# Optimization experiments

Measured on AMD Instinct MI355X. Metric: run time of the kernel, lower is better.

The kernel has to match this reference:

```python
import jax, jax.numpy as jnp
import numpy as np

N_NODES = 100000
N_EDGES = 1250000
D = 64  # in_dim == hid_dim (same Linear reused by both SSGConv layers)


def setup_inputs() -> dict:
    key = jax.random.key(0)
    k1, k2, k3, k4 = jax.random.split(key, 4)
    x = jax.random.normal(k1, (N_NODES, D), dtype=jnp.float32)
    edge_index = jax.random.randint(k2, (2, N_EDGES), 0, N_NODES, dtype=jnp.int64)
    W1 = jax.random.normal(k3, (D, D), dtype=jnp.float32) * (1.0 / np.sqrt(D))
    b1 = jax.random.normal(k4, (D,), dtype=jnp.float32) * 0.01
    return {"x": x, "edge_index": edge_index, "W1": W1, "b1": b1}


def reference(x, edge_index, W1, b1):
    # SSGConv(nn1): sum-aggregate neighbor features over edge_index, then Linear.
    src = edge_index[0]
    dst = edge_index[1]
    n = x.shape[0]

    def ssg_conv(h):
        # gather source-node features per edge, scatter-add into destinations
        agg = jax.ops.segment_sum(h[src], dst, num_segments=n)  # [N, D]
        return agg @ W1.T + b1  # shared nn1 for both layers (faithful to source)

    hid = ssg_conv(x)
    out = ssg_conv(hid)
    return (out, hid)
```

## Files before the change

### kernel.cpp

```cpp
#include <hip/hip_runtime.h>

#define N_NODES 100000
#define N_EDGES 1250000
#define D 64

#define BSHIFT 9
#define BUCKETS 196
#define CAP 8192
#define CHUNK 4096
#define PA_BLOCKS ((N_EDGES + CHUNK - 1) / CHUNK)
#define CVT_BLOCKS 718
#define LCAP 64

typedef long long ll;
typedef unsigned int uint;

__device__ __forceinline__ ushort f2bf(float f) {
    uint u = __float_as_uint(f);
    u += 0x7fffu + ((u >> 16) & 1u);
    return (ushort)(u >> 16);
}

__global__ void init_kernel(int* __restrict__ cursor, int* __restrict__ srt,
                            int* __restrict__ offs) {
    int t = threadIdx.x;
    if (t < BUCKETS) cursor[t] = t * CAP;
    if (t < 8) srt[N_EDGES + t] = 0;
    if (t == 0) offs[N_NODES] = N_EDGES;
}

__global__ __launch_bounds__(512) void bucketA_cvt_kernel(const int* __restrict__ src,
                                                          const int* __restrict__ dst,
                                                          int* __restrict__ cursor,
                                                          int* __restrict__ tmp,
                                                          const float* __restrict__ x,
                                                          ushort* __restrict__ xb) {
    int tid = threadIdx.x;
    if (blockIdx.x >= PA_BLOCKS) {
        const int n4 = N_NODES * D / 4;
        int i = (blockIdx.x - PA_BLOCKS) * 512 + tid;
        const int stride = CVT_BLOCKS * 512;
        for (; i < n4; i += stride) {
            float4 v = ((const float4*)x)[i];
            ushort4 o;
            o.x = f2bf(v.x); o.y = f2bf(v.y); o.z = f2bf(v.z); o.w = f2bf(v.w);
            ((ushort4*)xb)[i] = o;
        }
        return;
    }

    __shared__ int lcnt[BUCKETS];
    __shared__ int gbs[BUCKETS];
    __shared__ int list[BUCKETS * LCAP];
    if (tid < BUCKETS) lcnt[tid] = 0;
    __syncthreads();

    int base = blockIdx.x * CHUNK;
    int nE = min(CHUNK, N_EDGES - base);
    for (int i = tid; i < nE; i += 512) {
        int e = base + i;
        int s = src[e], d = dst[e];
        int b = d >> BSHIFT;
        int p = atomicAdd(&lcnt[b], 1);
        list[b * LCAP + p] = s | ((d & 511) << 17);
    }
    __syncthreads();

    if (tid < BUCKETS) gbs[tid] = atomicAdd(&cursor[tid], lcnt[tid]);
    __syncthreads();

    int wv = tid >> 6, lane = tid & 63;
    for (int b = wv; b < BUCKETS; b += 8) {
        int c = lcnt[b];
        if (lane < c) tmp[gbs[b] + lane] = list[b * LCAP + lane];
    }
}

__global__ __launch_bounds__(512) void bucketB_kernel(const int* __restrict__ cursor,
                                                      const int* __restrict__ tmp,
                                                      int* __restrict__ srt,
                                                      int* __restrict__ offs) {
    __shared__ int hist[512];
    __shared__ int cur[512];
    __shared__ int sbase[256];
    __shared__ int wsum[8];
    const int b = blockIdx.x, tid = threadIdx.x;
    const int wv = tid >> 6, lane = tid & 63;
    const int cbase = b * CAP;
    const int cnt = cursor[b] - cbase;

    hist[tid] = 0;
    if (wv == 0) {
        int c0, c1, c2, c3;
        const int b4 = lane << 2;
        c0 = (b4     < BUCKETS) ? (cursor[b4]     - (b4    ) * CAP) : 0;
        c1 = (b4 + 1 < BUCKETS) ? (cursor[b4 + 1] - (b4 + 1) * CAP) : 0;
        c2 = (b4 + 2 < BUCKETS) ? (cursor[b4 + 2] - (b4 + 2) * CAP) : 0;
        c3 = (b4 + 3 < BUCKETS) ? (cursor[b4 + 3] - (b4 + 3) * CAP) : 0;
        const int s1 = c0 + c1, sum = s1 + c2 + c3;
        int run = sum;
#pragma unroll
        for (int d = 1; d < 64; d <<= 1) {
            int t = __shfl_up(run, d);
            if (lane >= d) run += t;
        }
        const int lex = run - sum;
        sbase[b4]     = lex;
        sbase[b4 + 1] = lex + c0;
        sbase[b4 + 2] = lex + s1;
        sbase[b4 + 3] = lex + s1 + c2;
    }
    __syncthreads();
    const int gbase = sbase[b];

    for (int i = tid; i < cnt; i += 512) {
        int ln = tmp[cbase + i] >> 17;
        atomicAdd(&hist[ln], 1);
    }
    __syncthreads();

    const int x = hist[tid];
    int v = x;
#pragma unroll
    for (int d = 1; d < 64; d <<= 1) {
        int t = __shfl_up(v, d);
        if (lane >= d) v += t;
    }
    if (lane == 63) wsum[wv] = v;
    __syncthreads();
    int woff = 0;
#pragma unroll
    for (int k = 0; k < 8; ++k) woff += (k < wv) ? wsum[k] : 0;
    const int excl = v + woff - x;
    cur[tid] = excl;

    const int node0 = b << BSHIFT;
    const int nloc = min(512, N_NODES - node0);
    if (tid < nloc) offs[node0 + tid] = gbase + excl;
    __syncthreads();

    for (int i = tid; i < cnt; i += 512) {
        int t = tmp[cbase + i];
        int ln = t >> 17;
        int p = atomicAdd(&cur[ln], 1);
        srt[gbase + p] = t & 0x1FFFF;
    }
}

#define NBLK 2048
#define ACC4(P, M, AX, AY, AZ, AW)                        \
    {                                                     \
        float f0 = __uint_as_float((P).x << 16);          \
        float f1 = __uint_as_float((P).x & 0xffff0000u);  \
        float f2 = __uint_as_float((P).y << 16);          \
        float f3 = __uint_as_float((P).y & 0xffff0000u);  \
        AX = fmaf(f0, (M), AX); AY = fmaf(f1, (M), AY);   \
        AZ = fmaf(f2, (M), AZ); AW = fmaf(f3, (M), AW);   \
    }

template<int EMIT>
__global__ __launch_bounds__(256) void fused_layer(const ushort* __restrict__ hb,
                                                   const int* __restrict__ offs,
                                                   const int* __restrict__ srt,
                                                   const float* __restrict__ W1,
                                                   const float* __restrict__ b1,
                                                   float* __restrict__ out,
                                                   ushort* __restrict__ outb) {
    __shared__ __align__(16) float rbA[4][64];
    __shared__ __align__(16) float rbB[4][64];
    const int tid  = threadIdx.x;
    const int lane = tid & 63;
    const int wid  = tid >> 6;
    const int g    = lane >> 4;
    const int sub  = lane & 15;
    const uint roff = (uint)sub << 3;
    const int gw   = blockIdx.x * 4 + wid;
    const int GW   = NBLK * 4;
    const int goff = g << 2;
    const char* hbase = (const char*)hb;

    const float4* wrow = (const float4*)(W1 + lane * D);
    const float bj = b1[lane];

    for (int p = gw; p < (N_NODES >> 1); p += GW) {
        const int nA = p << 1;
        const int2 o2 = *(const int2*)(offs + nA);
        const int begA = o2.x;
        const int endA = o2.y;
        const int endB = offs[nA + 2];
        const int emA = (endA > begA) ? endA - 1 : begA;
        const int emB = (endB > endA) ? endB - 1 : endA;

        float aAx = 0.f, aAy = 0.f, aAz = 0.f, aAw = 0.f;
        float aBx = 0.f, aBy = 0.f, aBz = 0.f, aBw = 0.f;

        int ebA = begA, ebB = endA;
        while (ebA < endA || ebB < endB) {
            const int eA = ebA + goff;
            const int eB = ebB + goff;
            const int cA0 = min(eA,     emA), cA1 = min(eA + 1, emA);
            const int cA2 = min(eA + 2, emA), cA3 = min(eA + 3, emA);
            const int cB0 = min(eB,     emB), cB1 = min(eB + 1, emB);
            const int cB2 = min(eB + 2, emB), cB3 = min(eB + 3, emB);
            const int sA0 = srt[cA0];
            const int sA1 = srt[cA1];
            const int sA2 = srt[cA2];
            const int sA3 = srt[cA3];
            const int sB0 = srt[cB0];
            const int sB1 = srt[cB1];
            const int sB2 = srt[cB2];
            const int sB3 = srt[cB3];
            const uint2 vA0 = *(const uint2*)(hbase + (((uint)sA0 << 7) + roff));
            const uint2 vA1 = *(const uint2*)(hbase + (((uint)sA1 << 7) + roff));
            const uint2 vA2 = *(const uint2*)(hbase + (((uint)sA2 << 7) + roff));
            const uint2 vA3 = *(const uint2*)(hbase + (((uint)sA3 << 7) + roff));
            const uint2 vB0 = *(const uint2*)(hbase + (((uint)sB0 << 7) + roff));
            const uint2 vB1 = *(const uint2*)(hbase + (((uint)sB1 << 7) + roff));
            const uint2 vB2 = *(const uint2*)(hbase + (((uint)sB2 << 7) + roff));
            const uint2 vB3 = *(const uint2*)(hbase + (((uint)sB3 << 7) + roff));
            const float mA0 = (eA     < endA) ? 1.f : 0.f;
            const float mA1 = (eA + 1 < endA) ? 1.f : 0.f;
            const float mA2 = (eA + 2 < endA) ? 1.f : 0.f;
            const float mA3 = (eA + 3 < endA) ? 1.f : 0.f;
            const float mB0 = (eB     < endB) ? 1.f : 0.f;
            const float mB1 = (eB + 1 < endB) ? 1.f : 0.f;
            const float mB2 = (eB + 2 < endB) ? 1.f : 0.f;
            const float mB3 = (eB + 3 < endB) ? 1.f : 0.f;
            ACC4(vA0, mA0, aAx, aAy, aAz, aAw);
            ACC4(vA1, mA1, aAx, aAy, aAz, aAw);
            ACC4(vA2, mA2, aAx, aAy, aAz, aAw);
            ACC4(vA3, mA3, aAx, aAy, aAz, aAw);
            ACC4(vB0, mB0, aBx, aBy, aBz, aBw);
            ACC4(vB1, mB1, aBx, aBy, aBz, aBw);
            ACC4(vB2, mB2, aBx, aBy, aBz, aBw);
            ACC4(vB3, mB3, aBx, aBy, aBz, aBw);
            ebA += 16; ebB += 16;
        }

        aAx += __shfl_xor(aAx, 16); aAy += __shfl_xor(aAy, 16);
        aAz += __shfl_xor(aAz, 16); aAw += __shfl_xor(aAw, 16);
        aBx += __shfl_xor(aBx, 16); aBy += __shfl_xor(aBy, 16);
        aBz += __shfl_xor(aBz, 16); aBw += __shfl_xor(aBw, 16);
        aAx += __shfl_xor(aAx, 32); aAy += __shfl_xor(aAy, 32);
        aAz += __shfl_xor(aAz, 32); aAw += __shfl_xor(aAw, 32);
        aBx += __shfl_xor(aBx, 32); aBy += __shfl_xor(aBy, 32);
        aBz += __shfl_xor(aBz, 32); aBw += __shfl_xor(aBw, 32);

        if (g == 0) {
            float4 t; t.x = aAx; t.y = aAy; t.z = aAz; t.w = aAw;
            *((float4*)rbA[wid] + sub) = t;
        }
        if (g == 1) {
            float4 t; t.x = aBx; t.y = aBy; t.z = aBz; t.w = aBw;
            *((float4*)rbB[wid] + sub) = t;
        }

        float oA = bj, oB = bj;
        const float4* ra = (const float4*)rbA[wid];
        const float4* rb = (const float4*)rbB[wid];
#pragma unroll
        for (int k4 = 0; k4 < 16; ++k4) {
            const float4 w  = wrow[k4];
            const float4 rA = ra[k4];
            const float4 rB = rb[k4];
            oA += rA.x * w.x + rA.y * w.y + rA.z * w.z + rA.w * w.w;
            oB += rB.x * w.x + rB.y * w.y + rB.z * w.z + rB.w * w.w;
        }
        __builtin_nontemporal_store(oA, out + (ll)nA * D + lane);
        __builtin_nontemporal_store(oB, out + (ll)(nA + 1) * D + lane);
        if (EMIT) {
            outb[(ll)nA * D + lane]       = f2bf(oA);
            outb[(ll)(nA + 1) * D + lane] = f2bf(oB);
        }
    }
}

extern "C" void kernel_launch(void* const* d_in, const int* in_sizes, int n_in,
                              void* d_out, int out_size, void* d_ws, size_t ws_size,
                              hipStream_t stream) {
    const float* x  = (const float*)d_in[0];
    const int* edge = (const int*)d_in[1];
    const float* W1 = (const float*)d_in[2];
    const float* b1 = (const float*)d_in[3];

    const int* src = edge;
    const int* dst = edge + N_EDGES;

    float* out = (float*)d_out;
    float* hid = (float*)d_out + (ll)N_NODES * D;

    ushort* xb = (ushort*)d_out;

    char* ws = (char*)d_ws;
    int* cursor   = (int*)ws;  ws += 1024;
    int* offs     = (int*)ws;  ws += ((size_t)(N_NODES + 1) * 4 + 255) & ~255ull;
    int* srt      = (int*)ws;  ws += ((size_t)(N_EDGES + 8) * 4 + 255) & ~255ull;
    ushort* hidb  = (ushort*)ws; ws += (size_t)N_NODES * D * 2;
    int* tmp      = (int*)ws;

    init_kernel<<<1, 256, 0, stream>>>(cursor, srt, offs);
    bucketA_cvt_kernel<<<PA_BLOCKS + CVT_BLOCKS, 512, 0, stream>>>(src, dst, cursor,
                                                                   tmp, x, xb);
    bucketB_kernel<<<BUCKETS, 512, 0, stream>>>(cursor, tmp, srt, offs);

    fused_layer<1><<<NBLK, 256, 0, stream>>>(xb, offs, srt, W1, b1, hid, hidb);
    fused_layer<0><<<NBLK, 256, 0, stream>>>(hidb, offs, srt, W1, b1, out, (ushort*)nullptr);
}
```

Baseline: 230.4 us.

## Replace two-pass bucket sort with degree-count CSR padded to multiples of 16

```diff
diff --git a/kernel.cpp b/kernel.cpp
--- a/kernel.cpp
+++ b/kernel.cpp
@@ -6,11 +6,11 @@
 
 #define BSHIFT 9
 #define BUCKETS 196
-#define CAP 8192
-#define CHUNK 4096
-#define PA_BLOCKS ((N_EDGES + CHUNK - 1) / CHUNK)
+#define PAD_CAP 2400000
+#define CNT_BLOCKS 640
 #define CVT_BLOCKS 718
-#define LCAP 64
+#define SC_BLOCKS 1280
+#define NBLK 2048
 
 typedef long long ll;
 typedef unsigned int uint;
@@ -21,26 +21,32 @@
     return (ushort)(u >> 16);
 }
 
-__global__ void init_kernel(int* __restrict__ cursor, int* __restrict__ srt,
-                            int* __restrict__ offs) {
-    int t = threadIdx.x;
-    if (t < BUCKETS) cursor[t] = t * CAP;
-    if (t < 8) srt[N_EDGES + t] = 0;
-    if (t == 0) offs[N_NODES] = N_EDGES;
-}
-
-__global__ __launch_bounds__(512) void bucketA_cvt_kernel(const int* __restrict__ src,
-                                                          const int* __restrict__ dst,
-                                                          int* __restrict__ cursor,
-                                                          int* __restrict__ tmp,
-                                                          const float* __restrict__ x,
-                                                          ushort* __restrict__ xb) {
-    int tid = threadIdx.x;
-    if (blockIdx.x >= PA_BLOCKS) {
+__global__ __launch_bounds__(256) void prep_kernel(int* __restrict__ deg,
+                                                   int* __restrict__ srt,
+                                                   ushort* __restrict__ xb,
+                                                   ushort* __restrict__ hidb) {
+    const int i0 = blockIdx.x * 256 + threadIdx.x;
+    const int stride = gridDim.x * 256;
+    const int4 f4 = make_int4(N_NODES, N_NODES, N_NODES, N_NODES);
+    for (int i = i0; i < (PAD_CAP + 64) / 4; i += stride) ((int4*)srt)[i] = f4;
+    const int4 z4 = make_int4(0, 0, 0, 0);
+    for (int i = i0; i < N_NODES / 4; i += stride) ((int4*)deg)[i] = z4;
+    if (i0 < 16) {
+        uint2 z; z.x = 0; z.y = 0;
+        ((uint2*)(xb   + (ll)N_NODES * D))[i0] = z;
+        ((uint2*)(hidb + (ll)N_NODES * D))[i0] = z;
+    }
+}
+
+__global__ __launch_bounds__(512) void count_cvt_kernel(const int* __restrict__ dst,
+                                                        int* __restrict__ deg,
+                                                        const float* __restrict__ x,
+                                                        ushort* __restrict__ xb) {
+    const int tid = threadIdx.x;
+    if (blockIdx.x >= CNT_BLOCKS) {
         const int n4 = N_NODES * D / 4;
-        int i = (blockIdx.x - PA_BLOCKS) * 512 + tid;
-        const int stride = CVT_BLOCKS * 512;
-        for (; i < n4; i += stride) {
+        int i = (blockIdx.x - CNT_BLOCKS) * 512 + tid;
+        for (; i < n4; i += CVT_BLOCKS * 512) {
             float4 v = ((const float4*)x)[i];
             ushort4 o;
             o.x = f2bf(v.x); o.y = f2bf(v.y); o.z = f2bf(v.z); o.w = f2bf(v.w);
@@ -48,55 +54,47 @@
         }
         return;
     }
-
-    __shared__ int lcnt[BUCKETS];
-    __shared__ int gbs[BUCKETS];
-    __shared__ int list[BUCKETS * LCAP];
-    if (tid < BUCKETS) lcnt[tid] = 0;
+    int i = blockIdx.x * 512 + tid;
+    for (; i < N_EDGES; i += CNT_BLOCKS * 512) atomicAdd(&deg[dst[i]], 1);
+}
+
+__global__ __launch_bounds__(512) void degscan1_kernel(const int* __restrict__ deg,
+                                                       int* __restrict__ bsum) {
+    const int b = blockIdx.x, tid = threadIdx.x;
+    const int lane = tid & 63, wv = tid >> 6;
+    const int node0 = b << BSHIFT;
+    const int nloc = min(512, N_NODES - node0);
+    int pd = 0;
+    if (tid < nloc) pd = (deg[node0 + tid] + 15) & ~15;
+    int v = pd;
+#pragma unroll
+    for (int d = 1; d < 64; d <<= 1) v += __shfl_xor(v, d);
+    __shared__ int ws[8];
+    if (lane == 0) ws[wv] = v;
     __syncthreads();
-
-    int base = blockIdx.x * CHUNK;
-    int nE = min(CHUNK, N_EDGES - base);
-    for (int i = tid; i < nE; i += 512) {
-        int e = base + i;
-        int s = src[e], d = dst[e];
-        int b = d >> BSHIFT;
-        int p = atomicAdd(&lcnt[b], 1);
-        list[b * LCAP + p] = s | ((d & 511) << 17);
-    }
-    __syncthreads();
-
-    if (tid < BUCKETS) gbs[tid] = atomicAdd(&cursor[tid], lcnt[tid]);
-    __syncthreads();
-
-    int wv = tid >> 6, lane = tid & 63;
-    for (int b = wv; b < BUCKETS; b += 8) {
-        int c = lcnt[b];
-        if (lane < c) tmp[gbs[b] + lane] = list[b * LCAP + lane];
-    }
-}
-
-__global__ __launch_bounds__(512) void bucketB_kernel(const int* __restrict__ cursor,
-                                                      const int* __restrict__ tmp,
-                                                      int* __restrict__ srt,
-                                                      int* __restrict__ offs) {
-    __shared__ int hist[512];
-    __shared__ int cur[512];
+    if (tid == 0) {
+        int s = 0;
+#pragma unroll
+        for (int k = 0; k < 8; ++k) s += ws[k];
+        bsum[b] = s;
+    }
+}
+
+__global__ __launch_bounds__(512) void degscan2_kernel(const int* __restrict__ deg,
+                                                       const int* __restrict__ bsum,
+                                                       int* __restrict__ offs,
+                                                       int* __restrict__ cur) {
     __shared__ int sbase[256];
     __shared__ int wsum[8];
+    __shared__ int tot;
     const int b = blockIdx.x, tid = threadIdx.x;
-    const int wv = tid >> 6, lane = tid & 63;
-    const int cbase = b * CAP;
-    const int cnt = cursor[b] - cbase;
-
-    hist[tid] = 0;
+    const int lane = tid & 63, wv = tid >> 6;
     if (wv == 0) {
-        int c0, c1, c2, c3;
         const int b4 = lane << 2;
-        c0 = (b4     < BUCKETS) ? (cursor[b4]     - (b4    ) * CAP) : 0;
-        c1 = (b4 + 1 < BUCKETS) ? (cursor[b4 + 1] - (b4 + 1) * CAP) : 0;
-        c2 = (b4 + 2 < BUCKETS) ? (cursor[b4 + 2] - (b4 + 2) * CAP) : 0;
-        c3 = (b4 + 3 < BUCKETS) ? (cursor[b4 + 3] - (b4 + 3) * CAP) : 0;
+        int c0 = (b4     < BUCKETS) ? bsum[b4]     : 0;
+        int c1 = (b4 + 1 < BUCKETS) ? bsum[b4 + 1] : 0;
+        int c2 = (b4 + 2 < BUCKETS) ? bsum[b4 + 2] : 0;
+        int c3 = (b4 + 3 < BUCKETS) ? bsum[b4 + 3] : 0;
         const int s1 = c0 + c1, sum = s1 + c2 + c3;
         int run = sum;
 #pragma unroll
@@ -109,18 +107,14 @@
         sbase[b4 + 1] = lex + c0;
         sbase[b4 + 2] = lex + s1;
         sbase[b4 + 3] = lex + s1 + c2;
+        if (lane == 63) tot = run;
     }
     __syncthreads();
     const int gbase = sbase[b];
-
-    for (int i = tid; i < cnt; i += 512) {
-        int ln = tmp[cbase + i] >> 17;
-        atomicAdd(&hist[ln], 1);
-    }
-    __syncthreads();
-
-    const int x = hist[tid];
-    int v = x;
+    const int node0 = b << BSHIFT;
+    const int nloc = min(512, N_NODES - node0);
+    int pd = (tid < nloc) ? ((deg[node0 + tid] + 15) & ~15) : 0;
+    int v = pd;
 #pragma unroll
     for (int d = 1; d < 64; d <<= 1) {
         int t = __shfl_up(v, d);
@@ -131,32 +125,31 @@
     int woff = 0;
 #pragma unroll
     for (int k = 0; k < 8; ++k) woff += (k < wv) ? wsum[k] : 0;
-    const int excl = v + woff - x;
-    cur[tid] = excl;
-
-    const int node0 = b << BSHIFT;
-    const int nloc = min(512, N_NODES - node0);
-    if (tid < nloc) offs[node0 + tid] = gbase + excl;
-    __syncthreads();
-
-    for (int i = tid; i < cnt; i += 512) {
-        int t = tmp[cbase + i];
-        int ln = t >> 17;
-        int p = atomicAdd(&cur[ln], 1);
-        srt[gbase + p] = t & 0x1FFFF;
-    }
-}
-
-#define NBLK 2048
-#define ACC4(P, M, AX, AY, AZ, AW)                        \
-    {                                                     \
-        float f0 = __uint_as_float((P).x << 16);          \
-        float f1 = __uint_as_float((P).x & 0xffff0000u);  \
-        float f2 = __uint_as_float((P).y << 16);          \
-        float f3 = __uint_as_float((P).y & 0xffff0000u);  \
-        AX = fmaf(f0, (M), AX); AY = fmaf(f1, (M), AY);   \
-        AZ = fmaf(f2, (M), AZ); AW = fmaf(f3, (M), AW);   \
-    }
+    const int excl = v + woff - pd;
+    if (tid < nloc) {
+        offs[node0 + tid] = gbase + excl;
+        cur[node0 + tid]  = gbase + excl;
+    }
+    if (b == BUCKETS - 1 && tid == 0) offs[N_NODES] = tot;
+}
+
+__global__ __launch_bounds__(256) void scatter_kernel(const int* __restrict__ src,
+                                                      const int* __restrict__ dst,
+                                                      int* __restrict__ cur,
+                                                      int* __restrict__ srt) {
+    int i = blockIdx.x * 256 + threadIdx.x;
+    for (; i < N_EDGES; i += SC_BLOCKS * 256) {
+        int d = dst[i], s = src[i];
+        int p = atomicAdd(&cur[d], 1);
+        srt[p] = s;
+    }
+}
+
+#define UACC(V, AX, AY, AZ, AW)                               \
+    AX += __uint_as_float((V).x << 16);                       \
+    AY += __uint_as_float((V).x & 0xffff0000u);               \
+    AZ += __uint_as_float((V).y << 16);                       \
+    AW += __uint_as_float((V).y & 0xffff0000u);
 
 template<int EMIT>
 __global__ __launch_bounds__(256) void fused_layer(const ushort* __restrict__ hb,
@@ -174,9 +167,9 @@
     const int g    = lane >> 4;
     const int sub  = lane & 15;
     const uint roff = (uint)sub << 3;
+    const int goff = g << 2;
     const int gw   = blockIdx.x * 4 + wid;
     const int GW   = NBLK * 4;
-    const int goff = g << 2;
     const char* hbase = (const char*)hb;
 
     const float4* wrow = (const float4*)(W1 + lane * D);
@@ -188,52 +181,38 @@
         const int begA = o2.x;
         const int endA = o2.y;
         const int endB = offs[nA + 2];
-        const int emA = (endA > begA) ? endA - 1 : begA;
-        const int emB = (endB > endA) ? endB - 1 : endA;
 
         float aAx = 0.f, aAy = 0.f, aAz = 0.f, aAw = 0.f;
         float aBx = 0.f, aBy = 0.f, aBz = 0.f, aBw = 0.f;
 
         int ebA = begA, ebB = endA;
         while (ebA < endA || ebB < endB) {
-            const int eA = ebA + goff;
-            const int eB = ebB + goff;
-            const int cA0 = min(eA,     emA), cA1 = min(eA + 1, emA);
-            const int cA2 = min(eA + 2, emA), cA3 = min(eA + 3, emA);
-            const int cB0 = min(eB,     emB), cB1 = min(eB + 1, emB);
-            const int cB2 = min(eB + 2, emB), cB3 = min(eB + 3, emB);
-            const int sA0 = srt[cA0];
-            const int sA1 = srt[cA1];
-            const int sA2 = srt[cA2];
-            const int sA3 = srt[cA3];
-            const int sB0 = srt[cB0];
-            const int sB1 = srt[cB1];
-            const int sB2 = srt[cB2];
-            const int sB3 = srt[cB3];
-            const uint2 vA0 = *(const uint2*)(hbase + (((uint)sA0 << 7) + roff));
-            const uint2 vA1 = *(const uint2*)(hbase + (((uint)sA1 << 7) + roff));
-            const uint2 vA2 = *(const uint2*)(hbase + (((uint)sA2 << 7) + roff));
-            const uint2 vA3 = *(const uint2*)(hbase + (((uint)sA3 << 7) + roff));
-            const uint2 vB0 = *(const uint2*)(hbase + (((uint)sB0 << 7) + roff));
-            const uint2 vB1 = *(const uint2*)(hbase + (((uint)sB1 << 7) + roff));
-            const uint2 vB2 = *(const uint2*)(hbase + (((uint)sB2 << 7) + roff));
-            const uint2 vB3 = *(const uint2*)(hbase + (((uint)sB3 << 7) + roff));
-            const float mA0 = (eA     < endA) ? 1.f : 0.f;
-            const float mA1 = (eA + 1 < endA) ? 1.f : 0.f;
-            const float mA2 = (eA + 2 < endA) ? 1.f : 0.f;
-            const float mA3 = (eA + 3 < endA) ? 1.f : 0.f;
-            const float mB0 = (eB     < endB) ? 1.f : 0.f;
-            const float mB1 = (eB + 1 < endB) ? 1.f : 0.f;
-            const float mB2 = (eB + 2 < endB) ? 1.f : 0.f;
-            const float mB3 = (eB + 3 < endB) ? 1.f : 0.f;
-            ACC4(vA0, mA0, aAx, aAy, aAz, aAw);
-            ACC4(vA1, mA1, aAx, aAy, aAz, aAw);
-            ACC4(vA2, mA2, aAx, aAy, aAz, aAw);
-            ACC4(vA3, mA3, aAx, aAy, aAz, aAw);
-            ACC4(vB0, mB0, aBx, aBy, aBz, aBw);
-            ACC4(vB1, mB1, aBx, aBy, aBz, aBw);
-            ACC4(vB2, mB2, aBx, aBy, aBz, aBw);
-            ACC4(vB3, mB3, aBx, aBy, aBz, aBw);
+            int siA = (ebA < endA) ? srt[ebA + sub] : N_NODES;
+            int siB = (ebB < endB) ? srt[ebB + sub] : N_NODES;
+            const int iA0 = __shfl(siA, goff);
+            const int iA1 = __shfl(siA, goff + 1);
+            const int iA2 = __shfl(siA, goff + 2);
+            const int iA3 = __shfl(siA, goff + 3);
+            const int iB0 = __shfl(siB, goff);
+            const int iB1 = __shfl(siB, goff + 1);
+            const int iB2 = __shfl(siB, goff + 2);
+            const int iB3 = __shfl(siB, goff + 3);
+            const uint2 vA0 = *(const uint2*)(hbase + (((uint)iA0 << 7) + roff));
+            const uint2 vA1 = *(const uint2*)(hbase + (((uint)iA1 << 7) + roff));
+            const uint2 vA2 = *(const uint2*)(hbase + (((uint)iA2 << 7) + roff));
+            const uint2 vA3 = *(const uint2*)(hbase + (((uint)iA3 << 7) + roff));
+            const uint2 vB0 = *(const uint2*)(hbase + (((uint)iB0 << 7) + roff));
+            const uint2 vB1 = *(const uint2*)(hbase + (((uint)iB1 << 7) + roff));
+            const uint2 vB2 = *(const uint2*)(hbase + (((uint)iB2 << 7) + roff));
+            const uint2 vB3 = *(const uint2*)(hbase + (((uint)iB3 << 7) + roff));
+            UACC(vA0, aAx, aAy, aAz, aAw);
+            UACC(vA1, aAx, aAy, aAz, aAw);
+            UACC(vA2, aAx, aAy, aAz, aAw);
+            UACC(vA3, aAx, aAy, aAz, aAw);
+            UACC(vB0, aBx, aBy, aBz, aBw);
+            UACC(vB1, aBx, aBy, aBz, aBw);
+            UACC(vB2, aBx, aBy, aBz, aBw);
+            UACC(vB3, aBx, aBy, aBz, aBw);
             ebA += 16; ebB += 16;
         }
 
@@ -292,16 +271,18 @@
     ushort* xb = (ushort*)d_out;
 
     char* ws = (char*)d_ws;
-    int* cursor   = (int*)ws;  ws += 1024;
-    int* offs     = (int*)ws;  ws += ((size_t)(N_NODES + 1) * 4 + 255) & ~255ull;
-    int* srt      = (int*)ws;  ws += ((size_t)(N_EDGES + 8) * 4 + 255) & ~255ull;
-    ushort* hidb  = (ushort*)ws; ws += (size_t)N_NODES * D * 2;
-    int* tmp      = (int*)ws;
-
-    init_kernel<<<1, 256, 0, stream>>>(cursor, srt, offs);
-    bucketA_cvt_kernel<<<PA_BLOCKS + CVT_BLOCKS, 512, 0, stream>>>(src, dst, cursor,
-                                                                   tmp, x, xb);
-    bucketB_kernel<<<BUCKETS, 512, 0, stream>>>(cursor, tmp, srt, offs);
+    int* deg    = (int*)ws;  ws += ((size_t)N_NODES * 4 + 255) & ~255ull;
+    int* cur    = (int*)ws;  ws += ((size_t)N_NODES * 4 + 255) & ~255ull;
+    int* offs   = (int*)ws;  ws += ((size_t)(N_NODES + 1) * 4 + 255) & ~255ull;
+    int* bsum   = (int*)ws;  ws += 1024;
+    int* srt    = (int*)ws;  ws += ((size_t)(PAD_CAP + 64) * 4 + 255) & ~255ull;
+    ushort* hidb = (ushort*)ws;
+
+    prep_kernel<<<1024, 256, 0, stream>>>(deg, srt, xb, hidb);
+    count_cvt_kernel<<<CNT_BLOCKS + CVT_BLOCKS, 512, 0, stream>>>(dst, deg, x, xb);
+    degscan1_kernel<<<BUCKETS, 512, 0, stream>>>(deg, bsum);
+    degscan2_kernel<<<BUCKETS, 512, 0, stream>>>(deg, bsum, offs, cur);
+    scatter_kernel<<<SC_BLOCKS, 256, 0, stream>>>(src, dst, cur, srt);
 
     fused_layer<1><<<NBLK, 256, 0, stream>>>(xb, offs, srt, W1, b1, hid, hidb);
     fused_layer<0><<<NBLK, 256, 0, stream>>>(hidb, offs, srt, W1, b1, out, (ushort*)nullptr);
```

Result: slower. 334.0 us (+44.9%).
